# Kernel optimization log

Measured on AMD Instinct MI355X. Metric: run time of the kernel, lower is better.

The kernel has to match this reference:

```python
import jax, jax.numpy as jnp
import numpy as np

H = W = 56      # image resolution
WS = 7          # window size
SS = 3          # shift size
NH = 8          # num heads
E = 256         # embed dim
HD = E // NH    # head dim (qkv Linear operates per-head on HD)
NW = (H // WS) * (W // WS)  # 64 windows
WD = WS * WS                # 49 tokens per window


def _rel_pos_index():
    coords = np.stack(np.meshgrid(np.arange(WS), np.arange(WS), indexing='ij'))  # (2,WS,WS)
    cf = coords.reshape(2, -1)
    rel = (cf[:, :, None] - cf[:, None, :]).transpose(1, 2, 0)  # (WD,WD,2)
    rel[..., 0] += WS - 1
    rel[..., 1] += WS - 1
    rel[..., 0] *= 2 * WS - 1
    return rel.sum(-1)  # (WD,WD) ints in [0, (2WS-1)^2)


def _attn_mask():
    # Swin shifted-window attention mask: -100 where tokens come from different regions.
    m = np.zeros((H, W))
    slices = (slice(0, -WS), slice(-WS, -SS), slice(-SS, None))
    cnt = 0
    for hs in slices:
        for ws in slices:
            m[hs, ws] = cnt
            cnt += 1
    mw = m.reshape(H // WS, WS, W // WS, WS).transpose(0, 2, 1, 3).reshape(NW, WD)
    diff = mw[:, None, :] - mw[:, :, None]  # (NW,WD,WD)
    return np.where(diff != 0, -100.0, 0.0).astype(np.float32)


def setup_inputs() -> dict:
    key = jax.random.key(0)
    ks = jax.random.split(key, 6)
    return {
        'x': jax.random.normal(ks[0], (32, H * W, E), jnp.float32),
        'qkv_w': jax.random.normal(ks[1], (HD, 3 * HD), jnp.float32) * 0.05,
        'qkv_b': jax.random.normal(ks[2], (3 * HD,), jnp.float32) * 0.05,
        'proj_w': jax.random.normal(ks[3], (E, E), jnp.float32) * 0.05,
        'proj_b': jax.random.normal(ks[4], (E,), jnp.float32) * 0.05,
        'rpb_table': jax.random.normal(ks[5], ((2 * WS - 1) ** 2, NH), jnp.float32) * 0.02,
    }


def reference(x, qkv_w, qkv_b, proj_w, proj_b, rpb_table):
    B = x.shape[0]
    rpi = _rel_pos_index()
    bias = rpb_table[rpi.reshape(-1)].reshape(WD, WD, NH).transpose(2, 0, 1)  # (NH,WD,WD)
    mask = jnp.asarray(_attn_mask())  # (NW,WD,WD)

    xs = x.reshape(B, H, W, E)
    xs = jnp.roll(xs, (-SS, -SS), axis=(1, 2))  # cyclic shift (equals cycle_shift)
    # window partition -> (B,NW,WD,E)
    xw = xs.reshape(B, H // WS, WS, W // WS, WS, E).transpose(0, 1, 3, 2, 4, 5).reshape(B, NW, WD, E)
    # split heads -> (B,NW,NH,WD,HD)
    xh = xw.reshape(B, NW, WD, NH, HD).transpose(0, 1, 3, 2, 4)
    qkv = xh @ qkv_w + qkv_b  # per-head shared qkv projection (as in original)
    q, k, v = jnp.split(qkv, 3, axis=-1)
    scores = jnp.einsum('bwhqd,bwhkd->bwhqk', q, k) / np.sqrt(HD).astype(np.float32)
    scores = scores + bias + mask[None, :, None]  # (B,NW,NH,WD,WD)
    attn = jax.nn.softmax(scores, axis=-1)
    o = jnp.einsum('bwhqk,bwhkd->bwhqd', attn, v)
    # merge heads and reverse window partition
    o = o.transpose(0, 1, 3, 2, 4).reshape(B, NW, WD, E)
    o = o.reshape(B, H // WS, W // WS, WS, WS, E).transpose(0, 1, 3, 2, 4, 5).reshape(B, H, W, E)
    o = jnp.roll(o, (SS, SS), axis=(1, 2)).reshape(B, H * W, E)  # reverse cyclic shift
    return o @ proj_w + proj_b
```

## Files before the change

kernel.cpp:

```cpp
#include <hip/hip_runtime.h>
#include <hip/hip_bf16.h>

#define WSZ 7
#define WD  49
#define NH  8
#define NWIN 64
#define HH  56
#define SS  3
#define TOK 3136
#define EMB 256

typedef __attribute__((ext_vector_type(8))) short bf16x8;
typedef __attribute__((ext_vector_type(4))) float f32x4;

#define SWZ(row, col) ((col) ^ (((row) & 7) << 3))
#define PW_SH   10240
#define P_SH    4096
#define VT_SH   8192
#define LDS_TOTAL 81920
#define SO_STRIDE 264

__device__ __forceinline__ unsigned short f2bf(float f) {
    union { float f; unsigned u; } v; v.f = f;
    return (unsigned short)((v.u + 0x7FFFu + ((v.u >> 16) & 1u)) >> 16);
}
__device__ __forceinline__ unsigned cvt2p(float a, float b) {
    union { float f; unsigned u; } ua, ub;
    ua.f = a; ub.f = b;
    return __builtin_amdgcn_perm(ub.u + 0x8000u, ua.u + 0x8000u, 0x07060302u);
}
__device__ __forceinline__ unsigned long long pack4(float a, float b, float c, float d) {
    return (unsigned long long)cvt2p(a, b) | ((unsigned long long)cvt2p(c, d) << 32);
}

#define LOG2E 1.4426950408889634f

__global__ __launch_bounds__(256, 2) void fused_kernel(
    const float* __restrict__ x, const float* __restrict__ qkv_w,
    const float* __restrict__ qkv_b, const unsigned short* __restrict__ pWt,
    const float* __restrict__ proj_b, const float* __restrict__ tbl,
    float* __restrict__ out)
{
    extern __shared__ char smem[];

    const int tid = threadIdx.x;
    const int w = blockIdx.x & 63, b = blockIdx.x >> 6;
    const int wi = w >> 3, wj = w & 7;
    const int cls = (((wi == 7) ? 1 : 0) << 1) | ((wj == 7) ? 1 : 0);
    const int wave = tid >> 6, lane = tid & 63;
    const int cl = lane & 15, quad = lane >> 4;

    int pos4[4];
    #pragma unroll
    for (int mt = 0; mt < 4; ++mt) {
        int tok = mt * 16 + cl;
        int ti = (tok * 37) >> 8;
        int tj = tok - ti * 7;
        int r = wi * WSZ + ti + SS; if (r >= HH) r -= HH;
        int c = wj * WSZ + tj + SS; if (c >= HH) c -= HH;
        pos4[mt] = r * HH + c;
    }

    const float qscale = 0.17677669529663687f * LOG2E;
    f32x4 otr[2][2][4];

    {
        unsigned short* pwbase = (unsigned short*)smem + wave * PW_SH;
        unsigned short* __restrict__ sT  = pwbase;
        unsigned short* __restrict__ sP  = pwbase + P_SH;
        unsigned short* __restrict__ sVT = pwbase + VT_SH;

        bf16x8 xa2[2][4];
        #pragma unroll
        for (int mt = 0; mt < 4; ++mt) {
            const float* p = x + ((size_t)b * TOK + pos4[mt]) * EMB + quad * 8 + wave * 64;
            float4 v0 = *(const float4*)p;
            float4 v1 = *(const float4*)(p + 4);
            float4 v2 = *(const float4*)(p + 32);
            float4 v3 = *(const float4*)(p + 36);
            union { bf16x8 v; unsigned long long q[2]; } u0, u1;
            u0.q[0] = pack4(v0.x, v0.y, v0.z, v0.w);
            u0.q[1] = pack4(v1.x, v1.y, v1.z, v1.w);
            u1.q[0] = pack4(v2.x, v2.y, v2.z, v2.w);
            u1.q[1] = pack4(v3.x, v3.y, v3.z, v3.w);
            xa2[0][mt] = u0.v;
            xa2[1][mt] = u1.v;
        }

        bf16x8 wQK[4]; float4 bQK[4];
        #pragma unroll
        for (int mt = 0; mt < 4; ++mt) {
            const float* wp = qkv_w + quad * 8 * 96 + (mt * 16 + cl);
            union { bf16x8 v; unsigned long long q[2]; } u;
            u.q[0] = pack4(wp[0],   wp[96],  wp[192], wp[288]);
            u.q[1] = pack4(wp[384], wp[480], wp[576], wp[672]);
            wQK[mt] = u.v;
            bQK[mt] = *(const float4*)(qkv_b + mt * 16 + quad * 4);
        }
        bf16x8 wV[2]; float bV[2];
        #pragma unroll
        for (int i = 0; i < 2; ++i) {
            const float* wp = qkv_w + quad * 8 * 96 + (64 + i * 16 + cl);
            union { bf16x8 v; unsigned long long q[2]; } u;
            u.q[0] = pack4(wp[0],   wp[96],  wp[192], wp[288]);
            u.q[1] = pack4(wp[384], wp[480], wp[576], wp[672]);
            wV[i] = u.v;
            bV[i] = qkv_b[64 + i * 16 + cl];
        }

        #pragma unroll
        for (int hi = 0; hi < 2; ++hi) {
            const int h = wave * 2 + hi;
            #pragma unroll
            for (int mt = 0; mt < 4; ++mt) {
                #pragma unroll
                for (int nt = 0; nt < 4; ++nt) {
                    f32x4 c = {bQK[mt].x, bQK[mt].y, bQK[mt].z, bQK[mt].w};
                    c = __builtin_amdgcn_mfma_f32_16x16x32_bf16(wQK[mt], xa2[hi][nt], c, 0, 0, 0);
                    int tok = nt * 16 + cl;
                    if (mt < 2) {
                        int col0 = mt * 16 + quad * 4;
                        *(unsigned long long*)(&sT[tok * 64 + SWZ(tok, col0)]) =
                            pack4(c[0] * qscale, c[1] * qscale, c[2] * qscale, c[3] * qscale);
                    } else {
                        int col0 = 32 + (mt - 2) * 16 + quad * 4;
                        *(unsigned long long*)(&sT[tok * 64 + SWZ(tok, col0)]) =
                            pack4(c[0], c[1], c[2], c[3]);
                    }
                }
            }
            bf16x8 kb[4], qa[4];
            #pragma unroll
            for (int mt = 0; mt < 4; ++mt) {
                int rk = mt * 16 + cl;
                kb[mt] = *(const bf16x8*)(&sT[rk * 64 + SWZ(rk, 32 + quad * 8)]);
            }
            #pragma unroll
            for (int nt = 0; nt < 4; ++nt) {
                int rq = nt * 16 + cl;
                qa[nt] = *(const bf16x8*)(&sT[rq * 64 + SWZ(rq, quad * 8)]);
            }
            #pragma unroll
            for (int i = 0; i < 2; ++i) {
                #pragma unroll
                for (int mt = 0; mt < 4; ++mt) {
                    f32x4 c = {bV[i], bV[i], bV[i], bV[i]};
                    c = __builtin_amdgcn_mfma_f32_16x16x32_bf16(xa2[hi][mt], wV[i], c, 0, 0, 0);
                    int hd = i * 16 + cl;
                    *(unsigned long long*)(&sVT[hd * 64 + SWZ(hd, mt * 16 + quad * 4)]) =
                        pack4(c[0], c[1], c[2], c[3]);
                }
            }
            const float* tb = tbl + ((size_t)(cls * 8 + h) * 16) * 256 + lane * 4;
            f32x4 sc[4][4];
            #pragma unroll
            for (int mt = 0; mt < 4; ++mt)
                #pragma unroll
                for (int nt = 0; nt < 4; ++nt) {
                    f32x4 c = *(const f32x4*)(tb + (mt * 4 + nt) * 256);
                    sc[mt][nt] = __builtin_amdgcn_mfma_f32_16x16x32_bf16(kb[mt], qa[nt], c, 0, 0, 0);
                }
            #pragma unroll
            for (int nt = 0; nt < 4; ++nt) {
                float e[4][4];
                float sm = 0.f;
                #pragma unroll
                for (int mt = 0; mt < 4; ++mt)
                    #pragma unroll
                    for (int r = 0; r < 4; ++r) {
                        float v = __builtin_amdgcn_exp2f(sc[mt][nt][r]);
                        e[mt][r] = v; sm += v;
                    }
                sm += __shfl_xor(sm, 16);
                sm += __shfl_xor(sm, 32);
                float inv = 1.f / sm;
                int qt = nt * 16 + cl;
                #pragma unroll
                for (int mt = 0; mt < 4; ++mt)
                    *(unsigned long long*)(&sP[qt * 64 + SWZ(qt, mt * 16 + quad * 4)]) =
                        pack4(e[mt][0] * inv, e[mt][1] * inv, e[mt][2] * inv, e[mt][3] * inv);
            }
            #pragma unroll
            for (int mv = 0; mv < 2; ++mv)
                #pragma unroll
                for (int nt = 0; nt < 4; ++nt) otr[hi][mv][nt] = (f32x4){0.f, 0.f, 0.f, 0.f};
            #pragma unroll
            for (int ks = 0; ks < 2; ++ks) {
                bf16x8 va[2], pb[4];
                #pragma unroll
                for (int mv = 0; mv < 2; ++mv) {
                    int rv = mv * 16 + cl;
                    va[mv] = *(const bf16x8*)(&sVT[rv * 64 + SWZ(rv, ks * 32 + quad * 8)]);
                }
                #pragma unroll
                for (int nt = 0; nt < 4; ++nt) {
                    int rp = nt * 16 + cl;
                    pb[nt] = *(const bf16x8*)(&sP[rp * 64 + SWZ(rp, ks * 32 + quad * 8)]);
                }
                #pragma unroll
                for (int mv = 0; mv < 2; ++mv)
                    #pragma unroll
                    for (int nt = 0; nt < 4; ++nt)
                        otr[hi][mv][nt] = __builtin_amdgcn_mfma_f32_16x16x32_bf16(va[mv], pb[nt], otr[hi][mv][nt], 0, 0, 0);
            }
        }
    }

    __syncthreads();
    unsigned short* sO = (unsigned short*)smem;
    #pragma unroll
    for (int hi = 0; hi < 2; ++hi) {
        const int h = wave * 2 + hi;
        #pragma unroll
        for (int mv = 0; mv < 2; ++mv)
            #pragma unroll
            for (int nt = 0; nt < 4; ++nt) {
                int qt = nt * 16 + cl;
                f32x4 o = otr[hi][mv][nt];
                *(unsigned long long*)(&sO[qt * SO_STRIDE + h * 32 + mv * 16 + quad * 4]) =
                    pack4(o[0], o[1], o[2], o[3]);
            }
    }
    __syncthreads();

    const int n0 = wave * 64;
    f32x4 acc[4][4];
    #pragma unroll
    for (int mt = 0; mt < 4; ++mt)
        #pragma unroll
        for (int tt = 0; tt < 4; ++tt) acc[mt][tt] = (f32x4){0.f, 0.f, 0.f, 0.f};
    #pragma unroll
    for (int ks = 0; ks < 8; ++ks) {
        bf16x8 wa[4], ob[4];
        #pragma unroll
        for (int mt = 0; mt < 4; ++mt)
            wa[mt] = *(const bf16x8*)(pWt + (size_t)(((wave * 8 + ks) * 4 + mt) * 64 + lane) * 8);
        #pragma unroll
        for (int tt = 0; tt < 4; ++tt)
            ob[tt] = *(const bf16x8*)(&sO[(tt * 16 + cl) * SO_STRIDE + ks * 32 + quad * 8]);
        #pragma unroll
        for (int mt = 0; mt < 4; ++mt)
            #pragma unroll
            for (int tt = 0; tt < 4; ++tt)
                acc[mt][tt] = __builtin_amdgcn_mfma_f32_16x16x32_bf16(wa[mt], ob[tt], acc[mt][tt], 0, 0, 0);
    }
    #pragma unroll
    for (int mt = 0; mt < 4; ++mt) {
        float4 bq = *(const float4*)(proj_b + n0 + mt * 16 + quad * 4);
        #pragma unroll
        for (int tt = 0; tt < 4; ++tt) {
            int tok = tt * 16 + cl;
            if (tok < WD) {
                f32x4 v = acc[mt][tt];
                v[0] += bq.x; v[1] += bq.y; v[2] += bq.z; v[3] += bq.w;
                float* dst = out + ((size_t)b * TOK + pos4[tt]) * EMB + n0 + mt * 16 + quad * 4;
                *(f32x4*)dst = v;
            }
        }
    }
}

__global__ __launch_bounds__(256) void cvt_kernel(
    const float* __restrict__ W, unsigned short* __restrict__ Wt)
{
    int i = blockIdx.x * 256 + threadIdx.x;
    int k = i >> 8, n = i & 255;
    int wv = n >> 6, mt = (n >> 4) & 3, cl = n & 15;
    int ks = k >> 5, quad = (k >> 3) & 3, e = k & 7;
    Wt[(size_t)((((wv * 8 + ks) * 4 + mt) * 64) + quad * 16 + cl) * 8 + e] = f2bf(W[i]);
}

__global__ __launch_bounds__(256) void tbl_kernel(
    const float* __restrict__ rpb, float* __restrict__ tbl)
{
    int idx = blockIdx.x * 256 + threadIdx.x;
    int r = idx & 3;
    int lane = (idx >> 2) & 63;
    int cl = lane & 15, quad = lane >> 4;
    int tile = (idx >> 8) & 15;
    int mt = tile >> 2, nt = tile & 3;
    int h = (idx >> 12) & 7;
    int cls = (idx >> 15) & 3;
    int ci = cls >> 1, cj = cls & 1;

    int ktok = mt * 16 + quad * 4 + r;
    int qtok = nt * 16 + cl;

    float v;
    if (ktok >= WD) v = -1e30f;
    else if (qtok >= WD) v = 0.f;
    else {
        int qi = qtok / 7, qj = qtok - qi * 7;
        int ki = ktok / 7, kj = ktok - ki * 7;
        v = rpb[((qi - ki + 6) * 13 + (qj - kj + 6)) * NH + h];
        int qreg = (ci ? (qi < 4 ? 1 : 2) : 0) * 3 + (cj ? (qj < 4 ? 1 : 2) : 0);
        int kreg = (ci ? (ki < 4 ? 1 : 2) : 0) * 3 + (cj ? (kj < 4 ? 1 : 2) : 0);
        if (qreg != kreg) v -= 100.f;
    }
    tbl[idx] = v * 1.4426950408889634f;
}

extern "C" void kernel_launch(void* const* d_in, const int* in_sizes, int n_in,
                              void* d_out, int out_size, void* d_ws, size_t ws_size,
                              hipStream_t stream) {
    const float* x      = (const float*)d_in[0];
    const float* qkv_w  = (const float*)d_in[1];
    const float* qkv_b  = (const float*)d_in[2];
    const float* proj_w = (const float*)d_in[3];
    const float* proj_b = (const float*)d_in[4];
    const float* rpb    = (const float*)d_in[5];
    float* out = (float*)d_out;

    const int B = in_sizes[0] / (TOK * EMB);

    unsigned short* pWt = (unsigned short*)d_ws;
    float* tbl = (float*)((char*)d_ws + 131072);

    (void)hipFuncSetAttribute(reinterpret_cast<const void*>(&fused_kernel),
                              hipFuncAttributeMaxDynamicSharedMemorySize, LDS_TOTAL);
    cvt_kernel<<<256, 256, 0, stream>>>(proj_w, pWt);
    tbl_kernel<<<512, 256, 0, stream>>>(rpb, tbl);
    fused_kernel<<<B * NWIN, 256, LDS_TOTAL, stream>>>(x, qkv_w, qkv_b, pWt, proj_b, tbl, out);
}
```

Before: 240.4 us.

## Use one wave per head with 512-thread blocks in fused Swin attention

```diff
diff --git a/kernel.cpp b/kernel.cpp
--- a/kernel.cpp
+++ b/kernel.cpp
@@ -17,7 +17,7 @@
 #define PW_SH   10240
 #define P_SH    4096
 #define VT_SH   8192
-#define LDS_TOTAL 81920
+#define LDS_TOTAL 163840
 #define SO_STRIDE 264
 
 __device__ __forceinline__ unsigned short f2bf(float f) {
@@ -35,7 +35,7 @@
 
 #define LOG2E 1.4426950408889634f
 
-__global__ __launch_bounds__(256, 2) void fused_kernel(
+__global__ __launch_bounds__(512, 1) void fused_kernel(
     const float* __restrict__ x, const float* __restrict__ qkv_w,
     const float* __restrict__ qkv_b, const unsigned short* __restrict__ pWt,
     const float* __restrict__ proj_b, const float* __restrict__ tbl,
@@ -49,6 +49,7 @@
     const int cls = (((wi == 7) ? 1 : 0) << 1) | ((wj == 7) ? 1 : 0);
     const int wave = tid >> 6, lane = tid & 63;
     const int cl = lane & 15, quad = lane >> 4;
+    const int h = wave;
 
     int pos4[4];
     #pragma unroll
@@ -62,7 +63,7 @@
     }
 
     const float qscale = 0.17677669529663687f * LOG2E;
-    f32x4 otr[2][2][4];
+    f32x4 otr[2][4];
 
     {
         unsigned short* pwbase = (unsigned short*)smem + wave * PW_SH;
@@ -70,21 +71,16 @@
         unsigned short* __restrict__ sP  = pwbase + P_SH;
         unsigned short* __restrict__ sVT = pwbase + VT_SH;
 
-        bf16x8 xa2[2][4];
+        bf16x8 xa[4];
         #pragma unroll
         for (int mt = 0; mt < 4; ++mt) {
-            const float* p = x + ((size_t)b * TOK + pos4[mt]) * EMB + quad * 8 + wave * 64;
+            const float* p = x + ((size_t)b * TOK + pos4[mt]) * EMB + h * 32 + quad * 8;
             float4 v0 = *(const float4*)p;
             float4 v1 = *(const float4*)(p + 4);
-            float4 v2 = *(const float4*)(p + 32);
-            float4 v3 = *(const float4*)(p + 36);
-            union { bf16x8 v; unsigned long long q[2]; } u0, u1;
-            u0.q[0] = pack4(v0.x, v0.y, v0.z, v0.w);
-            u0.q[1] = pack4(v1.x, v1.y, v1.z, v1.w);
-            u1.q[0] = pack4(v2.x, v2.y, v2.z, v2.w);
-            u1.q[1] = pack4(v3.x, v3.y, v3.z, v3.w);
-            xa2[0][mt] = u0.v;
-            xa2[1][mt] = u1.v;
+            union { bf16x8 v; unsigned long long q[2]; } u;
+            u.q[0] = pack4(v0.x, v0.y, v0.z, v0.w);
+            u.q[1] = pack4(v1.x, v1.y, v1.z, v1.w);
+            xa[mt] = u.v;
         }
 
         bf16x8 wQK[4]; float4 bQK[4];
@@ -109,143 +105,135 @@
         }
 
         #pragma unroll
-        for (int hi = 0; hi < 2; ++hi) {
-            const int h = wave * 2 + hi;
-            #pragma unroll
-            for (int mt = 0; mt < 4; ++mt) {
-                #pragma unroll
-                for (int nt = 0; nt < 4; ++nt) {
-                    f32x4 c = {bQK[mt].x, bQK[mt].y, bQK[mt].z, bQK[mt].w};
-                    c = __builtin_amdgcn_mfma_f32_16x16x32_bf16(wQK[mt], xa2[hi][nt], c, 0, 0, 0);
-                    int tok = nt * 16 + cl;
-                    if (mt < 2) {
-                        int col0 = mt * 16 + quad * 4;
-                        *(unsigned long long*)(&sT[tok * 64 + SWZ(tok, col0)]) =
-                            pack4(c[0] * qscale, c[1] * qscale, c[2] * qscale, c[3] * qscale);
-                    } else {
-                        int col0 = 32 + (mt - 2) * 16 + quad * 4;
-                        *(unsigned long long*)(&sT[tok * 64 + SWZ(tok, col0)]) =
-                            pack4(c[0], c[1], c[2], c[3]);
-                    }
-                }
-            }
-            bf16x8 kb[4], qa[4];
-            #pragma unroll
-            for (int mt = 0; mt < 4; ++mt) {
-                int rk = mt * 16 + cl;
-                kb[mt] = *(const bf16x8*)(&sT[rk * 64 + SWZ(rk, 32 + quad * 8)]);
-            }
+        for (int mt = 0; mt < 4; ++mt) {
             #pragma unroll
             for (int nt = 0; nt < 4; ++nt) {
-                int rq = nt * 16 + cl;
-                qa[nt] = *(const bf16x8*)(&sT[rq * 64 + SWZ(rq, quad * 8)]);
-            }
-            #pragma unroll
-            for (int i = 0; i < 2; ++i) {
-                #pragma unroll
-                for (int mt = 0; mt < 4; ++mt) {
-                    f32x4 c = {bV[i], bV[i], bV[i], bV[i]};
-                    c = __builtin_amdgcn_mfma_f32_16x16x32_bf16(xa2[hi][mt], wV[i], c, 0, 0, 0);
-                    int hd = i * 16 + cl;
-                    *(unsigned long long*)(&sVT[hd * 64 + SWZ(hd, mt * 16 + quad * 4)]) =
+                f32x4 c = {bQK[mt].x, bQK[mt].y, bQK[mt].z, bQK[mt].w};
+                c = __builtin_amdgcn_mfma_f32_16x16x32_bf16(wQK[mt], xa[nt], c, 0, 0, 0);
+                int tok = nt * 16 + cl;
+                if (mt < 2) {
+                    int col0 = mt * 16 + quad * 4;
+                    *(unsigned long long*)(&sT[tok * 64 + SWZ(tok, col0)]) =
+                        pack4(c[0] * qscale, c[1] * qscale, c[2] * qscale, c[3] * qscale);
+                } else {
+                    int col0 = 32 + (mt - 2) * 16 + quad * 4;
+                    *(unsigned long long*)(&sT[tok * 64 + SWZ(tok, col0)]) =
                         pack4(c[0], c[1], c[2], c[3]);
                 }
             }
-            const float* tb = tbl + ((size_t)(cls * 8 + h) * 16) * 256 + lane * 4;
-            f32x4 sc[4][4];
+        }
+        bf16x8 kb[4], qa[4];
+        #pragma unroll
+        for (int mt = 0; mt < 4; ++mt) {
+            int rk = mt * 16 + cl;
+            kb[mt] = *(const bf16x8*)(&sT[rk * 64 + SWZ(rk, 32 + quad * 8)]);
+        }
+        #pragma unroll
+        for (int nt = 0; nt < 4; ++nt) {
+            int rq = nt * 16 + cl;
+            qa[nt] = *(const bf16x8*)(&sT[rq * 64 + SWZ(rq, quad * 8)]);
+        }
+        #pragma unroll
+        for (int i = 0; i < 2; ++i) {
+            #pragma unroll
+            for (int mt = 0; mt < 4; ++mt) {
+                f32x4 c = {bV[i], bV[i], bV[i], bV[i]};
+                c = __builtin_amdgcn_mfma_f32_16x16x32_bf16(xa[mt], wV[i], c, 0, 0, 0);
+                int hd = i * 16 + cl;
+                *(unsigned long long*)(&sVT[hd * 64 + SWZ(hd, mt * 16 + quad * 4)]) =
+                    pack4(c[0], c[1], c[2], c[3]);
+            }
+        }
+        const float* tb = tbl + ((size_t)(cls * 8 + h) * 16) * 256 + lane * 4;
+        f32x4 sc[4][4];
+        #pragma unroll
+        for (int mt = 0; mt < 4; ++mt)
+            #pragma unroll
+            for (int nt = 0; nt < 4; ++nt) {
+                f32x4 c = *(const f32x4*)(tb + (mt * 4 + nt) * 256);
+                sc[mt][nt] = __builtin_amdgcn_mfma_f32_16x16x32_bf16(kb[mt], qa[nt], c, 0, 0, 0);
+            }
+        #pragma unroll
+        for (int nt = 0; nt < 4; ++nt) {
+            float e[4][4];
+            float sm = 0.f;
             #pragma unroll
             for (int mt = 0; mt < 4; ++mt)
                 #pragma unroll
-                for (int nt = 0; nt < 4; ++nt) {
-                    f32x4 c = *(const f32x4*)(tb + (mt * 4 + nt) * 256);
-                    sc[mt][nt] = __builtin_amdgcn_mfma_f32_16x16x32_bf16(kb[mt], qa[nt], c, 0, 0, 0);
+                for (int r = 0; r < 4; ++r) {
+                    float v = __builtin_amdgcn_exp2f(sc[mt][nt][r]);
+                    e[mt][r] = v; sm += v;
                 }
+            sm += __shfl_xor(sm, 16);
+            sm += __shfl_xor(sm, 32);
+            float inv = 1.f / sm;
+            int qt = nt * 16 + cl;
+            #pragma unroll
+            for (int mt = 0; mt < 4; ++mt)
+                *(unsigned long long*)(&sP[qt * 64 + SWZ(qt, mt * 16 + quad * 4)]) =
+                    pack4(e[mt][0] * inv, e[mt][1] * inv, e[mt][2] * inv, e[mt][3] * inv);
+        }
+        #pragma unroll
+        for (int mv = 0; mv < 2; ++mv)
+            #pragma unroll
+            for (int nt = 0; nt < 4; ++nt) otr[mv][nt] = (f32x4){0.f, 0.f, 0.f, 0.f};
+        #pragma unroll
+        for (int ks = 0; ks < 2; ++ks) {
+            bf16x8 va[2], pb[4];
+            #pragma unroll
+            for (int mv = 0; mv < 2; ++mv) {
+                int rv = mv * 16 + cl;
+                va[mv] = *(const bf16x8*)(&sVT[rv * 64 + SWZ(rv, ks * 32 + quad * 8)]);
+            }
             #pragma unroll
             for (int nt = 0; nt < 4; ++nt) {
-                float e[4][4];
-                float sm = 0.f;
-                #pragma unroll
-                for (int mt = 0; mt < 4; ++mt)
-                    #pragma unroll
-                    for (int r = 0; r < 4; ++r) {
-                        float v = __builtin_amdgcn_exp2f(sc[mt][nt][r]);
-                        e[mt][r] = v; sm += v;
-                    }
-                sm += __shfl_xor(sm, 16);
-                sm += __shfl_xor(sm, 32);
-                float inv = 1.f / sm;
-                int qt = nt * 16 + cl;
-                #pragma unroll
-                for (int mt = 0; mt < 4; ++mt)
-                    *(unsigned long long*)(&sP[qt * 64 + SWZ(qt, mt * 16 + quad * 4)]) =
-                        pack4(e[mt][0] * inv, e[mt][1] * inv, e[mt][2] * inv, e[mt][3] * inv);
+                int rp = nt * 16 + cl;
+                pb[nt] = *(const bf16x8*)(&sP[rp * 64 + SWZ(rp, ks * 32 + quad * 8)]);
             }
             #pragma unroll
             for (int mv = 0; mv < 2; ++mv)
                 #pragma unroll
-                for (int nt = 0; nt < 4; ++nt) otr[hi][mv][nt] = (f32x4){0.f, 0.f, 0.f, 0.f};
-            #pragma unroll
-            for (int ks = 0; ks < 2; ++ks) {
-                bf16x8 va[2], pb[4];
-                #pragma unroll
-                for (int mv = 0; mv < 2; ++mv) {
-                    int rv = mv * 16 + cl;
-                    va[mv] = *(const bf16x8*)(&sVT[rv * 64 + SWZ(rv, ks * 32 + quad * 8)]);
-                }
-                #pragma unroll
-                for (int nt = 0; nt < 4; ++nt) {
-                    int rp = nt * 16 + cl;
-                    pb[nt] = *(const bf16x8*)(&sP[rp * 64 + SWZ(rp, ks * 32 + quad * 8)]);
-                }
-                #pragma unroll
-                for (int mv = 0; mv < 2; ++mv)
-                    #pragma unroll
-                    for (int nt = 0; nt < 4; ++nt)
-                        otr[hi][mv][nt] = __builtin_amdgcn_mfma_f32_16x16x32_bf16(va[mv], pb[nt], otr[hi][mv][nt], 0, 0, 0);
-            }
+                for (int nt = 0; nt < 4; ++nt)
+                    otr[mv][nt] = __builtin_amdgcn_mfma_f32_16x16x32_bf16(va[mv], pb[nt], otr[mv][nt], 0, 0, 0);
         }
     }
 
     __syncthreads();
     unsigned short* sO = (unsigned short*)smem;
     #pragma unroll
-    for (int hi = 0; hi < 2; ++hi) {
-        const int h = wave * 2 + hi;
-        #pragma unroll
-        for (int mv = 0; mv < 2; ++mv)
-            #pragma unroll
-            for (int nt = 0; nt < 4; ++nt) {
-                int qt = nt * 16 + cl;
-                f32x4 o = otr[hi][mv][nt];
-                *(unsigned long long*)(&sO[qt * SO_STRIDE + h * 32 + mv * 16 + quad * 4]) =
-                    pack4(o[0], o[1], o[2], o[3]);
-            }
-    }
+    for (int mv = 0; mv < 2; ++mv)
+        #pragma unroll
+        for (int nt = 0; nt < 4; ++nt) {
+            int qt = nt * 16 + cl;
+            f32x4 o = otr[mv][nt];
+            *(unsigned long long*)(&sO[qt * SO_STRIDE + h * 32 + mv * 16 + quad * 4]) =
+                pack4(o[0], o[1], o[2], o[3]);
+        }
     __syncthreads();
 
-    const int n0 = wave * 64;
-    f32x4 acc[4][4];
-    #pragma unroll
-    for (int mt = 0; mt < 4; ++mt)
+    const int n0 = wave * 32;
+    f32x4 acc[2][4];
+    #pragma unroll
+    for (int mt = 0; mt < 2; ++mt)
         #pragma unroll
         for (int tt = 0; tt < 4; ++tt) acc[mt][tt] = (f32x4){0.f, 0.f, 0.f, 0.f};
     #pragma unroll
     for (int ks = 0; ks < 8; ++ks) {
-        bf16x8 wa[4], ob[4];
-        #pragma unroll
-        for (int mt = 0; mt < 4; ++mt)
-            wa[mt] = *(const bf16x8*)(pWt + (size_t)(((wave * 8 + ks) * 4 + mt) * 64 + lane) * 8);
+        bf16x8 wa[2], ob[4];
+        #pragma unroll
+        for (int mt = 0; mt < 2; ++mt)
+            wa[mt] = *(const bf16x8*)(pWt + (size_t)(((wave * 8 + ks) * 2 + mt) * 64 + lane) * 8);
         #pragma unroll
         for (int tt = 0; tt < 4; ++tt)
             ob[tt] = *(const bf16x8*)(&sO[(tt * 16 + cl) * SO_STRIDE + ks * 32 + quad * 8]);
         #pragma unroll
-        for (int mt = 0; mt < 4; ++mt)
+        for (int mt = 0; mt < 2; ++mt)
             #pragma unroll
             for (int tt = 0; tt < 4; ++tt)
                 acc[mt][tt] = __builtin_amdgcn_mfma_f32_16x16x32_bf16(wa[mt], ob[tt], acc[mt][tt], 0, 0, 0);
     }
     #pragma unroll
-    for (int mt = 0; mt < 4; ++mt) {
+    for (int mt = 0; mt < 2; ++mt) {
         float4 bq = *(const float4*)(proj_b + n0 + mt * 16 + quad * 4);
         #pragma unroll
         for (int tt = 0; tt < 4; ++tt) {
@@ -265,9 +253,9 @@
 {
     int i = blockIdx.x * 256 + threadIdx.x;
     int k = i >> 8, n = i & 255;
-    int wv = n >> 6, mt = (n >> 4) & 3, cl = n & 15;
+    int wv = n >> 5, mt = (n >> 4) & 1, cl = n & 15;
     int ks = k >> 5, quad = (k >> 3) & 3, e = k & 7;
-    Wt[(size_t)((((wv * 8 + ks) * 4 + mt) * 64) + quad * 16 + cl) * 8 + e] = f2bf(W[i]);
+    Wt[(size_t)((((wv * 8 + ks) * 2 + mt) * 64) + quad * 16 + cl) * 8 + e] = f2bf(W[i]);
 }
 
 __global__ __launch_bounds__(256) void tbl_kernel(
@@ -320,5 +308,5 @@
                               hipFuncAttributeMaxDynamicSharedMemorySize, LDS_TOTAL);
     cvt_kernel<<<256, 256, 0, stream>>>(proj_w, pWt);
     tbl_kernel<<<512, 256, 0, stream>>>(rpb, tbl);
-    fused_kernel<<<B * NWIN, 256, LDS_TOTAL, stream>>>(x, qkv_w, qkv_b, pWt, proj_b, tbl, out);
-}
+    fused_kernel<<<B * NWIN, 512, LDS_TOTAL, stream>>>(x, qkv_w, qkv_b, pWt, proj_b, tbl, out);
+}
```

Measured after the change: 242.4 us. Within noise of the previous version (+0.8%).
